# Kernel optimization log

Hardware: AMD Instinct MI355X
Metric: run time of the kernel (lower is better)

## Reference

```python
import jax, jax.numpy as jnp
import numpy as np

D_IN = 1024
D_OUT = 1024
D_BOT = 512


def setup_inputs() -> dict:
    key = jax.random.key(0)
    ks = jax.random.split(key, 16)
    B, Sq, Skv = 8, 2048, 2048

    def lin(k, fan_in, fan_out):
        kw, kb = jax.random.split(k)
        bound = 1.0 / np.sqrt(fan_in)
        W = jax.random.uniform(kw, (fan_in, fan_out), jnp.float32, -bound, bound)
        b = jax.random.uniform(kb, (fan_out,), jnp.float32, -bound, bound)
        return W, b

    W1, b1 = lin(ks[0], D_IN, D_IN)
    W2, b2 = lin(ks[1], D_IN, D_BOT)
    W3, b3 = lin(ks[2], D_BOT, D_IN)
    W4, b4 = lin(ks[3], D_IN, D_IN)
    Wq, bq = lin(ks[4], D_IN, D_OUT)
    Wk, bk = lin(ks[5], D_IN, D_OUT)
    Wv, bv = lin(ks[6], D_IN, D_OUT)

    x = jax.random.normal(ks[7], (B, Sq, D_IN), jnp.float32)
    y = jax.random.normal(ks[8], (B, Skv, D_IN), jnp.float32)
    return {
        "x": x, "y": y,
        "W1": W1, "b1": b1, "W2": W2, "b2": b2,
        "W3": W3, "b3": b3, "W4": W4, "b4": b4,
        "Wq": Wq, "bq": bq, "Wk": Wk, "bk": bk, "Wv": Wv, "bv": bv,
    }


def reference(x, y, W1, b1, W2, b2, W3, b3, W4, b4, Wq, bq, Wk, bk, Wv, bv):
    # 4-layer MLP with ReLU after every linear
    h = jax.nn.relu(x @ W1 + b1)
    h = jax.nn.relu(h @ W2 + b2)
    h = jax.nn.relu(h @ W3 + b3)
    h = jax.nn.relu(h @ W4 + b4)
    # cross-attention projections
    q = h @ Wq + bq          # [B, Sq, D_OUT]
    k = y @ Wk + bk          # [B, Skv, D_OUT]
    v = y @ Wv + bv          # [B, Skv, D_OUT]
    scale = 1.0 / jnp.sqrt(jnp.float32(q.shape[-1]))
    scores = jnp.einsum('bqd,bkd->bqk', q, k) * scale  # [B, Sq, Skv]
    attn_w = jax.nn.softmax(scores, axis=-1)
    out = jnp.einsum('bqk,bkd->bqd', attn_w, v)
    return out
```

## Files before the change

kernel.cpp:

```cpp
#include <hip/hip_runtime.h>
#include <stdint.h>


typedef __attribute__((ext_vector_type(8))) short bf16x8;
typedef __attribute__((ext_vector_type(4))) float f32x4;
typedef __attribute__((ext_vector_type(8))) unsigned short u16x8;

__device__ __forceinline__ float bf2f(unsigned short u) {
    return __uint_as_float(((unsigned int)u) << 16);
}
__device__ __forceinline__ unsigned short f2bf(float f) {
    unsigned int u = __float_as_uint(f);
    unsigned int r = (u + 0x7fffu + ((u >> 16) & 1u)) >> 16;
    return (unsigned short)r;
}

__device__ __forceinline__ void async16(const void* g, void* l) {
    __builtin_amdgcn_global_load_lds(
        (const __attribute__((address_space(1))) unsigned int*)g,
        (__attribute__((address_space(3))) unsigned int*)l,
        16, 0, 0);
}

__global__ __launch_bounds__(64) void detect_dtype(
    const unsigned short* __restrict__ w, int* __restrict__ flag)
{
    const int t = threadIdx.x;
    int cnt = 0;
    for (int i = t; i < 4096; i += 64) {
        const unsigned e = (w[i] >> 7) & 0xFF;
        cnt += (e >= 140) ? 1 : 0;
    }
#pragma unroll
    for (int off = 32; off; off >>= 1) cnt += __shfl_xor(cnt, off, 64);
    if (t == 0) flag[0] = (cnt >= 8) ? 1 : 0;
}

__global__ __launch_bounds__(256) void conv_bias_all(
    const void* b1, const void* b2, const void* b3, const void* b4,
    const void* bq, const void* bk, const void* bv,
    float* __restrict__ out, const int* __restrict__ flag)
{
    const int i = blockIdx.x * 256 + threadIdx.x;
    const int slot = i >> 10, idx = i & 1023;
    if (slot == 1 && idx >= 512) return;
    const void* src = (slot == 0) ? b1 : (slot == 1) ? b2 : (slot == 2) ? b3 :
                      (slot == 3) ? b4 : (slot == 4) ? bq : (slot == 5) ? bk : bv;
    out[i] = (*flag) ? ((const float*)src)[idx]
                     : bf2f(((const unsigned short*)src)[idx]);
}

__device__ __forceinline__ void wt_body(
    const void* in, unsigned short* out, int R, int C, int f)
{
    __shared__ unsigned short tile[32][33];
    const int bc = blockIdx.x * 32;
    const int br = blockIdx.y * 32;
    const int x = threadIdx.x & 31;
    const int y = threadIdx.x >> 5;
#pragma unroll
    for (int i = 0; i < 4; i++) {
        const int r = y + i * 8;
        unsigned short v;
        if (f) v = f2bf(((const float*)in)[(size_t)(br + r) * C + bc + x]);
        else   v = ((const unsigned short*)in)[(size_t)(br + r) * C + bc + x];
        tile[r][x] = v;
    }
    __syncthreads();
#pragma unroll
    for (int i = 0; i < 4; i++) {
        const int r = y + i * 8;
        out[(size_t)(bc + r) * R + br + x] = tile[x][r];
    }
}

__global__ __launch_bounds__(256) void conv_weight_t7(
    const void* i0, unsigned short* o0, const void* i1, unsigned short* o1,
    const void* i2, unsigned short* o2, const void* i3, unsigned short* o3,
    const void* i4, unsigned short* o4, const void* i5, unsigned short* o5,
    const void* i6, unsigned short* o6, const int* flag)
{
    const int z = blockIdx.z;
    if (z == 5) {
        if (blockIdx.x >= 16) return;
        wt_body(i5, o5, 1024, 512, *flag);
        return;
    }
    if (z == 6) {
        if (blockIdx.y >= 16) return;
        wt_body(i6, o6, 512, 1024, *flag);
        return;
    }
    const void* in = (z == 0) ? i0 : (z == 1) ? i1 : (z == 2) ? i2 : (z == 3) ? i3 : i4;
    unsigned short* out = (z == 0) ? o0 : (z == 1) ? o1 : (z == 2) ? o2 : (z == 3) ? o3 : o4;
    wt_body(in, out, 1024, 1024, *flag);
}

__global__ __launch_bounds__(256) void conv_to_bf16(
    const void* __restrict__ in, unsigned short* __restrict__ out,
    int n, const int* __restrict__ flag)
{
    const int i = (blockIdx.x * 256 + threadIdx.x) * 8;
    if (i >= n) return;
    if (*flag) {
        const float4* p = (const float4*)((const float*)in + i);
        const float4 a = p[0], b = p[1];
        u16x8 o;
        o[0] = f2bf(a.x); o[1] = f2bf(a.y); o[2] = f2bf(a.z); o[3] = f2bf(a.w);
        o[4] = f2bf(b.x); o[5] = f2bf(b.y); o[6] = f2bf(b.z); o[7] = f2bf(b.w);
        *(u16x8*)(out + i) = o;
    } else {
        *(u16x8*)(out + i) = *(const u16x8*)((const unsigned short*)in + i);
    }
}

__global__ __launch_bounds__(256) void write_out(
    const unsigned short* __restrict__ src, void* __restrict__ dst,
    int n, const int* __restrict__ flag)
{
    const int i = (blockIdx.x * 256 + threadIdx.x) * 8;
    if (i >= n) return;
    const u16x8 v = *(const u16x8*)(src + i);
    if (*flag) {
        float4 a, b;
        a.x = bf2f(v[0]); a.y = bf2f(v[1]); a.z = bf2f(v[2]); a.w = bf2f(v[3]);
        b.x = bf2f(v[4]); b.y = bf2f(v[5]); b.z = bf2f(v[6]); b.w = bf2f(v[7]);
        float4* p = (float4*)((float*)dst + i);
        p[0] = a; p[1] = b;
    } else {
        *(u16x8*)((unsigned short*)dst + i) = v;
    }
}

template <int RELU, int BIAS, int OUTF, int SWZ>
__global__ __launch_bounds__(256, 2) void gemm_bt(
    const unsigned short* __restrict__ A, const unsigned short* __restrict__ B,
    const float* __restrict__ bias, void* __restrict__ C,
    int M, int N, int K, float alpha,
    long long sA, long long sB, long long sC, const int* __restrict__ flag)
{
    int bxi = blockIdx.x, byi = blockIdx.y;
    if (SWZ) {
        const int id = byi * gridDim.x + bxi;
        bxi = (id >> 3) % gridDim.x;
        byi = (id >> 3) / gridDim.x * 8 + (id & 7);
    }
    const int z = blockIdx.z;
    A += (size_t)z * (size_t)sA;
    B += (size_t)z * (size_t)sB;
    const size_t cofs = (size_t)z * (size_t)sC;

    const int bm = byi * 128;
    const int bn = bxi * 128;
    const int t = threadIdx.x;
    const int lane = t & 63;
    const int w = t >> 6;
    const int wr = (w >> 1) * 64;
    const int wc = (w & 1) * 64;

    __shared__ unsigned short sAt[128 * 32];
    __shared__ unsigned short sBt[128 * 32];

    f32x4 acc[4][4];
#pragma unroll
    for (int i = 0; i < 4; i++)
#pragma unroll
        for (int j = 0; j < 4; j++)
            acc[i][j] = (f32x4){0.f, 0.f, 0.f, 0.f};

    const int tr = t >> 2;
    const int tc = (t & 3) << 3;
    const unsigned short* ga = A + (size_t)(bm + tr) * K + tc;
    const unsigned short* gb = B + (size_t)(bn + tr) * K + tc;
    unsigned short* la = &sAt[tr * 32 + tc];
    unsigned short* lb = &sBt[tr * 32 + tc];

    const int am = wr + (lane & 15);
    const int bn_ = wc + (lane & 15);
    const int ak = (lane >> 4) * 8;

    for (int k0 = 0; k0 < K; k0 += 32) {
        async16(ga, la);
        async16(ga + (size_t)64 * K, la + 64 * 32);
        async16(gb, lb);
        async16(gb + (size_t)64 * K, lb + 64 * 32);
        ga += 32;
        gb += 32;
        __syncthreads();

        bf16x8 af[4], bfr[4];
#pragma unroll
        for (int i = 0; i < 4; i++)
            af[i] = *(const bf16x8*)&sAt[(am + i * 16) * 32 + ak];
#pragma unroll
        for (int j = 0; j < 4; j++)
            bfr[j] = *(const bf16x8*)&sBt[(bn_ + j * 16) * 32 + ak];
#pragma unroll
        for (int i = 0; i < 4; i++)
#pragma unroll
            for (int j = 0; j < 4; j++)
                acc[i][j] = __builtin_amdgcn_mfma_f32_16x16x32_bf16(
                    af[i], bfr[j], acc[i][j], 0, 0, 0);
        __syncthreads();
    }

    const int fl = OUTF ? *flag : 0;
#pragma unroll
    for (int i = 0; i < 4; i++) {
        const int row0 = bm + wr + i * 16 + (lane >> 4) * 4;
#pragma unroll
        for (int j = 0; j < 4; j++) {
            const int col = bn + wc + j * 16 + (lane & 15);
            float bc = 0.f;
            if (BIAS == 1) bc = bias[col];
#pragma unroll
            for (int r = 0; r < 4; r++) {
                float bv = bc;
                if (BIAS == 2) bv = bias[row0 + r];
                float vv = acc[i][j][r] * alpha + bv;
                if (RELU) vv = fmaxf(vv, 0.f);
                const size_t idx = cofs + (size_t)(row0 + r) * N + col;
                if (OUTF && fl) ((float*)C)[idx] = vv;
                else ((unsigned short*)C)[idx] = f2bf(vv);
            }
        }
    }
}

#define G8_STG(gbase, dbase, T, h) do {                                        \
    const unsigned short* _s = (gbase) + (size_t)((h) * 128) * K               \
                                       + (size_t)(T) * 64;                     \
    unsigned short* _d = (dbase) + (((T) & 1) ? 16384 : 0) + (h) * 8192;       \
    async16(_s, _d);                                                           \
    async16(_s + (size_t)64 * K, _d + 4096);                                   \
} while (0)

#define G8_RD_LO(PA_, PB_)                                                     \
    _Pragma("unroll")                                                          \
    for (int m_ = 0; m_ < 4; m_++) {                                           \
        aL[m_][0] = *(const bf16x8*)&(PA_)[rA + m_ * 1024 + c0];               \
        aL[m_][1] = *(const bf16x8*)&(PA_)[rA + m_ * 1024 + c1];               \
    }                                                                          \
    _Pragma("unroll")                                                          \
    for (int n_ = 0; n_ < 4; n_++)                                             \
        bb[n_][0] = *(const bf16x8*)&(PB_)[rB + n_ * 1024 + c0];

#define G8_RD_HI(PA_, PB_)                                                     \
    _Pragma("unroll")                                                          \
    for (int m_ = 0; m_ < 4; m_++) {                                           \
        aH[m_][0] = *(const bf16x8*)&(PA_)[rA + (m_ + 4) * 1024 + c0];         \
        aH[m_][1] = *(const bf16x8*)&(PA_)[rA + (m_ + 4) * 1024 + c1];         \
    }                                                                          \
    _Pragma("unroll")                                                          \
    for (int n_ = 0; n_ < 4; n_++)                                             \
        bb[n_][1] = *(const bf16x8*)&(PB_)[rB + n_ * 1024 + c1];

#define G8_TOP()                                                               \
    __builtin_amdgcn_s_barrier();                                              \
    asm volatile("s_waitcnt lgkmcnt(0)" ::: "memory");                         \
    __builtin_amdgcn_sched_barrier(0);                                         \
    __builtin_amdgcn_s_setprio(1);

#define G8_FMA(AF, KK, MOFS)                                                   \
    _Pragma("unroll")                                                          \
    for (int m_ = 0; m_ < 4; m_++) {                                           \
        _Pragma("unroll")                                                      \
        for (int n_ = 0; n_ < 4; n_++)                                         \
            acc[(MOFS) + m_][n_] = __builtin_amdgcn_mfma_f32_16x16x32_bf16(    \
                AF[m_][KK], bb[n_][KK], acc[(MOFS) + m_][n_], 0, 0, 0);        \
    }

#define G8_BOT()                                                               \
    __builtin_amdgcn_s_setprio(0);                                             \
    asm volatile("" ::: "memory");                                             \
    __builtin_amdgcn_s_barrier();                                              \
    asm volatile("" ::: "memory");

#define G8_BOTVM4()                                                            \
    __builtin_amdgcn_s_setprio(0);                                             \
    asm volatile("s_waitcnt vmcnt(4)" ::: "memory");                           \
    __builtin_amdgcn_s_barrier();                                              \
    asm volatile("" ::: "memory");

#define G8_BOTVM0()                                                            \
    __builtin_amdgcn_s_setprio(0);                                             \
    asm volatile("s_waitcnt vmcnt(0)" ::: "memory");                           \
    __builtin_amdgcn_s_barrier();                                              \
    asm volatile("" ::: "memory");

template <int RELU, int BIAS, int OUTF, int SWZ>
__global__ __launch_bounds__(512, 2) void gemm8(
    const unsigned short* __restrict__ A, const unsigned short* __restrict__ B,
    const float* __restrict__ bias, void* __restrict__ C,
    int M, int N, int K, float alpha,
    long long sA, long long sB, long long sC, const int* __restrict__ flag)
{
    extern __shared__ unsigned short lds[];
    (void)M;
    int bxi = blockIdx.x, byi = blockIdx.y;
    if (SWZ) {
        const int id = byi * gridDim.x + bxi;
        bxi = (id >> 3) % gridDim.x;
        byi = (id >> 3) / gridDim.x * 8 + (id & 7);
    }
    const int z = blockIdx.z;
    A += (size_t)z * (size_t)sA;
    B += (size_t)z * (size_t)sB;
    const size_t cofs = (size_t)z * (size_t)sC;

    const int bm = byi * 256;
    const int bn = bxi * 256;
    const int t = threadIdx.x;
    const int lane = t & 63;
    const int w = t >> 6;
    const int wm = w >> 2;
    const int wn = w & 3;

    unsigned short* LA = lds;
    unsigned short* LB = lds + 32768;

    const int rowi = t >> 3;
    const int co = ((t & 7) ^ (rowi & 7)) << 3;
    const unsigned short* gA = A + (size_t)(bm + rowi) * K + co;
    const unsigned short* gB = B + (size_t)(bn + rowi) * K + co;
    unsigned short* dA = LA + t * 8;
    unsigned short* dB = LB + t * 8;

    const int rA = (wm * 128 + (lane & 15)) * 64;
    const int rB = (wn * 64 + (lane & 15)) * 64;
    const int swz = (lane & 7) << 4;
    const int c0 = ((((lane >> 4) << 4)) ^ swz) >> 1;
    const int c1 = ((64 | ((lane >> 4) << 4)) ^ swz) >> 1;

    f32x4 acc[8][4];
#pragma unroll
    for (int i = 0; i < 8; i++)
#pragma unroll
        for (int j = 0; j < 4; j++)
            acc[i][j] = (f32x4){0.f, 0.f, 0.f, 0.f};

    bf16x8 aL[4][2], aH[4][2], bb[4][2];

    G8_STG(gA, dA, 0, 0);
    G8_STG(gA, dA, 0, 1);
    G8_STG(gB, dB, 0, 0);
    G8_STG(gB, dB, 0, 1);
    G8_STG(gA, dA, 1, 0);
    G8_STG(gA, dA, 1, 1);
    asm volatile("s_waitcnt vmcnt(4)" ::: "memory");
    __builtin_amdgcn_s_barrier();
    asm volatile("" ::: "memory");

    const int NI = K >> 7;
    int kt = 0;
    for (int i = 0; i < NI - 1; ++i, kt += 2) {
        G8_RD_LO(LA, LB)
        G8_STG(gB, dB, kt + 1, 0);
        G8_TOP()
        G8_FMA(aL, 0, 0)
        G8_BOT()
        G8_RD_HI(LA, LB)
        G8_STG(gB, dB, kt + 1, 1);
        G8_TOP()
        G8_FMA(aL, 1, 0)
        G8_BOT()
        G8_STG(gA, dA, kt + 2, 0);
        G8_TOP()
        G8_FMA(aH, 0, 4)
        G8_BOT()
        G8_STG(gA, dA, kt + 2, 1);
        G8_TOP()
        G8_FMA(aH, 1, 4)
        G8_BOTVM4()
        G8_RD_LO((LA + 16384), (LB + 16384))
        G8_STG(gB, dB, kt + 2, 0);
        G8_TOP()
        G8_FMA(aL, 0, 0)
        G8_BOT()
        G8_RD_HI((LA + 16384), (LB + 16384))
        G8_STG(gB, dB, kt + 2, 1);
        G8_TOP()
        G8_FMA(aL, 1, 0)
        G8_BOT()
        G8_STG(gA, dA, kt + 3, 0);
        G8_TOP()
        G8_FMA(aH, 0, 4)
        G8_BOT()
        G8_STG(gA, dA, kt + 3, 1);
        G8_TOP()
        G8_FMA(aH, 1, 4)
        G8_BOTVM4()
    }
    {
        G8_RD_LO(LA, LB)
        G8_STG(gB, dB, kt + 1, 0);
        G8_TOP()
        G8_FMA(aL, 0, 0)
        G8_BOT()
        G8_RD_HI(LA, LB)
        G8_STG(gB, dB, kt + 1, 1);
        G8_TOP()
        G8_FMA(aL, 1, 0)
        G8_BOT()
        G8_TOP()
        G8_FMA(aH, 0, 4)
        G8_BOT()
        G8_TOP()
        G8_FMA(aH, 1, 4)
        G8_BOTVM0()
        G8_RD_LO((LA + 16384), (LB + 16384))
        G8_TOP()
        G8_FMA(aL, 0, 0)
        G8_BOT()
        G8_RD_HI((LA + 16384), (LB + 16384))
        G8_TOP()
        G8_FMA(aL, 1, 0)
        G8_BOT()
        G8_TOP()
        G8_FMA(aH, 0, 4)
        G8_BOT()
        G8_TOP()
        G8_FMA(aH, 1, 4)
        __builtin_amdgcn_s_setprio(0);
    }

    const int fl = OUTF ? *flag : 0;
#pragma unroll
    for (int mi = 0; mi < 8; mi++) {
        const int row0 = bm + wm * 128 + mi * 16 + (lane >> 4) * 4;
#pragma unroll
        for (int n = 0; n < 4; n++) {
            const int col = bn + wn * 64 + n * 16 + (lane & 15);
            float bc = 0.f;
            if (BIAS == 1) bc = bias[col];
#pragma unroll
            for (int r = 0; r < 4; r++) {
                float bv = bc;
                if (BIAS == 2) bv = bias[row0 + r];
                float vv = acc[mi][n][r] * alpha + bv;
                if (RELU) vv = fmaxf(vv, 0.f);
                const size_t idx = cofs + (size_t)(row0 + r) * N + col;
                if (OUTF && fl) ((float*)C)[idx] = vv;
                else ((unsigned short*)C)[idx] = f2bf(vv);
            }
        }
    }
}

__global__ __launch_bounds__(256) void softmax_rows(unsigned short* S, int n)
{
    const size_t row = blockIdx.x;
    unsigned short* p = S + row * (size_t)n;
    const int t = threadIdx.x;
    const int lane = t & 63;
    const int wave = t >> 6;

    u16x8 v = *(const u16x8*)(p + t * 8);
    float f[8];
    float m = -3.0e38f;
#pragma unroll
    for (int i = 0; i < 8; i++) {
        f[i] = bf2f(v[i]);
        m = fmaxf(m, f[i]);
    }
#pragma unroll
    for (int off = 32; off; off >>= 1) m = fmaxf(m, __shfl_xor(m, off, 64));
    __shared__ float redm[4];
    if (lane == 0) redm[wave] = m;
    __syncthreads();
    m = fmaxf(fmaxf(redm[0], redm[1]), fmaxf(redm[2], redm[3]));

    float e[8];
    float s = 0.f;
#pragma unroll
    for (int i = 0; i < 8; i++) {
        e[i] = __expf(f[i] - m);
        s += e[i];
    }
#pragma unroll
    for (int off = 32; off; off >>= 1) s += __shfl_xor(s, off, 64);
    __shared__ float reds[4];
    if (lane == 0) reds[wave] = s;
    __syncthreads();
    s = reds[0] + reds[1] + reds[2] + reds[3];
    const float inv = 1.0f / s;

    u16x8 o;
#pragma unroll
    for (int i = 0; i < 8; i++) o[i] = f2bf(e[i] * inv);
    *(u16x8*)(p + t * 8) = o;
}

extern "C" void kernel_launch(void* const* d_in, const int* in_sizes, int n_in,
                              void* d_out, int out_size, void* d_ws, size_t ws_size,
                              hipStream_t stream)
{
    const void* x  = d_in[0];
    const void* y  = d_in[1];
    const void* W1 = d_in[2];
    const void* b1 = d_in[3];
    const void* W2 = d_in[4];
    const void* b2 = d_in[5];
    const void* W3 = d_in[6];
    const void* b3 = d_in[7];
    const void* W4 = d_in[8];
    const void* b4 = d_in[9];
    const void* Wq = d_in[10];
    const void* bq = d_in[11];
    const void* Wk = d_in[12];
    const void* bk = d_in[13];
    const void* Wv = d_in[14];
    const void* bv = d_in[15];

    int* flag = (int*)d_ws;
    float* fb = (float*)((char*)d_ws + 64);
    unsigned short* arena = (unsigned short*)((char*)d_ws + 64 + 7 * 1024 * 4);
    const size_t baseB = 64 + 7 * 1024 * 4;
    const size_t MEG = 1024ull * 1024ull;

    auto needB = [&](int G, bool direct) -> size_t {
        return baseB + 2ull * ((6 + 16 + (size_t)G * 6 + (direct ? 0 : 16)) * MEG);
    };
    int G; bool direct;
    if (ws_size >= needB(8, true))      { G = 8; direct = true;  }
    else if (ws_size >= needB(4, false)) { G = 4; direct = false; }
    else if (ws_size >= needB(2, false)) { G = 2; direct = false; }
    else                                 { G = 1; direct = false; }

    unsigned short* W1t = arena;
    unsigned short* W2t = W1t + 1 * MEG;
    unsigned short* W3t = W2t + MEG / 2;
    unsigned short* W4t = W3t + MEG / 2;
    unsigned short* Wqt = W4t + 1 * MEG;
    unsigned short* Wkt = Wqt + 1 * MEG;
    unsigned short* Wvt = Wkt + 1 * MEG;
    unsigned short* XC  = Wvt + 1 * MEG;
    unsigned short* VT  = XC + 16 * MEG;
    unsigned short* SBUF = VT + (size_t)G * 2 * MEG;
    unsigned short* OUTS = SBUF + (size_t)G * 4 * MEG;

    unsigned short* PA = (unsigned short*)d_out;
    unsigned short* PB = PA + 16 * MEG;

    float* fb1 = fb;
    float* fb2 = fb + 1024;
    float* fb3 = fb + 2048;
    float* fb4 = fb + 3072;
    float* fbq = fb + 4096;
    float* fbk = fb + 5120;
    float* fbv = fb + 6144;

    const dim3 blk(256);
    const dim3 blk8(512);
    const int LDS8 = 131072;
    const int NE = 16 * 1024 * 1024;
    const int Mx = 16384;
    const long long Z0 = 0;
    const long long sQK = 2048ll * 1024;
    const long long sS  = 2048ll * 2048;

    (void)hipFuncSetAttribute((const void*)&gemm8<1, 1, 0, 1>,
                              hipFuncAttributeMaxDynamicSharedMemorySize, LDS8);
    (void)hipFuncSetAttribute((const void*)&gemm8<0, 1, 0, 1>,
                              hipFuncAttributeMaxDynamicSharedMemorySize, LDS8);
    (void)hipFuncSetAttribute((const void*)&gemm8<0, 2, 0, 0>,
                              hipFuncAttributeMaxDynamicSharedMemorySize, LDS8);
    (void)hipFuncSetAttribute((const void*)&gemm8<0, 0, 0, 1>,
                              hipFuncAttributeMaxDynamicSharedMemorySize, LDS8);
    (void)hipFuncSetAttribute((const void*)&gemm8<0, 0, 1, 1>,
                              hipFuncAttributeMaxDynamicSharedMemorySize, LDS8);

    detect_dtype<<<1, 64, 0, stream>>>((const unsigned short*)W1, flag);
    conv_bias_all<<<28, blk, 0, stream>>>(b1, b2, b3, b4, bq, bk, bv, fb, flag);
    conv_weight_t7<<<dim3(32, 32, 7), blk, 0, stream>>>(
        W1, W1t, W4, W4t, Wq, Wqt, Wk, Wkt, Wv, Wvt, W2, W2t, W3, W3t, flag);

    conv_to_bf16<<<8192, blk, 0, stream>>>(x, XC, NE, flag);

    gemm8<1, 1, 0, 1><<<dim3(4, 64), blk8, LDS8, stream>>>(
        XC, W1t, fb1, PA, Mx, 1024, 1024, 1.f, Z0, Z0, Z0, flag);
    gemm_bt<1, 1, 0, 1><<<dim3(4, 128), blk, 0, stream>>>(
        PA, W2t, fb2, PB, Mx, 512, 1024, 1.f, Z0, Z0, Z0, flag);
    gemm8<1, 1, 0, 1><<<dim3(4, 64), blk8, LDS8, stream>>>(
        PB, W3t, fb3, PA, Mx, 1024, 512, 1.f, Z0, Z0, Z0, flag);
    gemm8<1, 1, 0, 1><<<dim3(4, 64), blk8, LDS8, stream>>>(
        PA, W4t, fb4, PB, Mx, 1024, 1024, 1.f, Z0, Z0, Z0, flag);

    gemm8<0, 1, 0, 1><<<dim3(4, 64), blk8, LDS8, stream>>>(
        PB, Wqt, fbq, PA, Mx, 1024, 1024, 1.f, Z0, Z0, Z0, flag);
    conv_to_bf16<<<8192, blk, 0, stream>>>(y, XC, NE, flag);
    gemm8<0, 1, 0, 1><<<dim3(4, 64), blk8, LDS8, stream>>>(
        XC, Wkt, fbk, PB, Mx, 1024, 1024, 1.f, Z0, Z0, Z0, flag);

    if (direct) {
        gemm8<0, 2, 0, 0><<<dim3(8, 4, 8), blk8, LDS8, stream>>>(
            Wvt, XC, fbv, VT, 1024, 2048, 1024, 1.f, Z0, sQK, sQK, flag);
        gemm8<0, 0, 0, 1><<<dim3(8, 8, 8), blk8, LDS8, stream>>>(
            PA, PB, nullptr, SBUF, 2048, 2048, 1024, 0.03125f, sQK, sQK, sS, flag);
        softmax_rows<<<dim3(8 * 2048), blk, 0, stream>>>(SBUF, 2048);
        gemm8<0, 0, 1, 1><<<dim3(4, 8, 8), blk8, LDS8, stream>>>(
            SBUF, VT, nullptr, d_out, 2048, 1024, 2048, 1.f, sS, sQK, sQK, flag);
    } else {
        for (int g = 0; g < 8; g += G) {
            const size_t off = (size_t)g * 2048 * 1024;
            gemm_bt<0, 2, 0, 0><<<dim3(16, 8, G), blk, 0, stream>>>(
                Wvt, XC + off, fbv, VT, 1024, 2048, 1024, 1.f, Z0, sQK, sQK, flag);
            gemm_bt<0, 0, 0, 1><<<dim3(16, 16, G), blk, 0, stream>>>(
                PA + off, PB + off, nullptr, SBUF, 2048, 2048, 1024, 0.03125f, sQK, sQK, sS, flag);
            softmax_rows<<<dim3(G * 2048), blk, 0, stream>>>(SBUF, 2048);
            gemm_bt<0, 0, 0, 1><<<dim3(8, 16, G), blk, 0, stream>>>(
                SBUF, VT, nullptr, OUTS + off, 2048, 1024, 2048, 1.f, sS, sQK, sQK, flag);
        }
        write_out<<<8192, blk, 0, stream>>>(OUTS, d_out, NE, flag);
    }
}
```

Before: 621.1 us.

## Split LDS fragment reads and use partial lgkmcnt waits in gemm8 pipeline

Splits the LDS fragment reads into ordered groups separated by sched_barriers. Each MFMA phase now waits only for the fragments it needs (partial lgkmcnt counts) instead of draining all LDS reads. It also restructures the global-to-LDS staging so the B tile for the next k-step is issued in the prologue and alongside A in later phases, with vmcnt adjusted to match. This is meant to overlap LDS reads with MFMA work, at the cost of relying on exact hand-counted waitcnt values being correct.

Measured after the change: 793.7 us. 1.28x slower.

```diff
diff --git a/kernel.cpp b/kernel.cpp
--- a/kernel.cpp
+++ b/kernel.cpp
@@ -235,29 +235,34 @@
     async16(_s + (size_t)64 * K, _d + 4096);                                   \
 } while (0)
 
-#define G8_RD_LO(PA_, PB_)                                                     \
+#define G8_RDA(PA_, PB_)                                                       \
     _Pragma("unroll")                                                          \
-    for (int m_ = 0; m_ < 4; m_++) {                                           \
+    for (int m_ = 0; m_ < 4; m_++)                                             \
         aL[m_][0] = *(const bf16x8*)&(PA_)[rA + m_ * 1024 + c0];               \
-        aL[m_][1] = *(const bf16x8*)&(PA_)[rA + m_ * 1024 + c1];               \
-    }                                                                          \
     _Pragma("unroll")                                                          \
     for (int n_ = 0; n_ < 4; n_++)                                             \
-        bb[n_][0] = *(const bf16x8*)&(PB_)[rB + n_ * 1024 + c0];
-
-#define G8_RD_HI(PA_, PB_)                                                     \
+        bb[n_][0] = *(const bf16x8*)&(PB_)[rB + n_ * 1024 + c0];               \
+    __builtin_amdgcn_sched_barrier(0);                                         \
     _Pragma("unroll")                                                          \
-    for (int m_ = 0; m_ < 4; m_++) {                                           \
-        aH[m_][0] = *(const bf16x8*)&(PA_)[rA + (m_ + 4) * 1024 + c0];         \
-        aH[m_][1] = *(const bf16x8*)&(PA_)[rA + (m_ + 4) * 1024 + c1];         \
-    }                                                                          \
+    for (int m_ = 0; m_ < 4; m_++)                                             \
+        aL[m_][1] = *(const bf16x8*)&(PA_)[rA + m_ * 1024 + c1];
+
+#define G8_RDB(PA_, PB_)                                                       \
     _Pragma("unroll")                                                          \
     for (int n_ = 0; n_ < 4; n_++)                                             \
-        bb[n_][1] = *(const bf16x8*)&(PB_)[rB + n_ * 1024 + c1];
-
-#define G8_TOP()                                                               \
+        bb[n_][1] = *(const bf16x8*)&(PB_)[rB + n_ * 1024 + c1];               \
+    __builtin_amdgcn_sched_barrier(0);                                         \
+    _Pragma("unroll")                                                          \
+    for (int m_ = 0; m_ < 4; m_++)                                             \
+        aH[m_][0] = *(const bf16x8*)&(PA_)[rA + (m_ + 4) * 1024 + c0];         \
+    __builtin_amdgcn_sched_barrier(0);                                         \
+    _Pragma("unroll")                                                          \
+    for (int m_ = 0; m_ < 4; m_++)                                             \
+        aH[m_][1] = *(const bf16x8*)&(PA_)[rA + (m_ + 4) * 1024 + c1];
+
+#define G8_TOP(LG)                                                             \
     __builtin_amdgcn_s_barrier();                                              \
-    asm volatile("s_waitcnt lgkmcnt(0)" ::: "memory");                         \
+    asm volatile("s_waitcnt lgkmcnt(" #LG ")" ::: "memory");                   \
     __builtin_amdgcn_sched_barrier(0);                                         \
     __builtin_amdgcn_s_setprio(1);
 
@@ -276,15 +281,9 @@
     __builtin_amdgcn_s_barrier();                                              \
     asm volatile("" ::: "memory");
 
-#define G8_BOTVM4()                                                            \
+#define G8_BOTVM(N)                                                            \
     __builtin_amdgcn_s_setprio(0);                                             \
-    asm volatile("s_waitcnt vmcnt(4)" ::: "memory");                           \
-    __builtin_amdgcn_s_barrier();                                              \
-    asm volatile("" ::: "memory");
-
-#define G8_BOTVM0()                                                            \
-    __builtin_amdgcn_s_setprio(0);                                             \
-    asm volatile("s_waitcnt vmcnt(0)" ::: "memory");                           \
+    asm volatile("s_waitcnt vmcnt(" #N ")" ::: "memory");                      \
     __builtin_amdgcn_s_barrier();                                              \
     asm volatile("" ::: "memory");
 
@@ -347,79 +346,79 @@
     G8_STG(gB, dB, 0, 1);
     G8_STG(gA, dA, 1, 0);
     G8_STG(gA, dA, 1, 1);
-    asm volatile("s_waitcnt vmcnt(4)" ::: "memory");
+    G8_STG(gB, dB, 1, 0);
+    G8_STG(gB, dB, 1, 1);
+    asm volatile("s_waitcnt vmcnt(8)" ::: "memory");
     __builtin_amdgcn_s_barrier();
     asm volatile("" ::: "memory");
 
     const int NI = K >> 7;
     int kt = 0;
     for (int i = 0; i < NI - 1; ++i, kt += 2) {
-        G8_RD_LO(LA, LB)
-        G8_STG(gB, dB, kt + 1, 0);
-        G8_TOP()
+        G8_RDA(LA, LB)
+        G8_TOP(4)
         G8_FMA(aL, 0, 0)
         G8_BOT()
-        G8_RD_HI(LA, LB)
-        G8_STG(gB, dB, kt + 1, 1);
-        G8_TOP()
+        G8_RDB(LA, LB)
+        G8_TOP(8)
         G8_FMA(aL, 1, 0)
         G8_BOT()
         G8_STG(gA, dA, kt + 2, 0);
-        G8_TOP()
+        G8_STG(gB, dB, kt + 2, 0);
+        G8_TOP(4)
         G8_FMA(aH, 0, 4)
         G8_BOT()
         G8_STG(gA, dA, kt + 2, 1);
-        G8_TOP()
+        G8_STG(gB, dB, kt + 2, 1);
+        G8_TOP(0)
         G8_FMA(aH, 1, 4)
-        G8_BOTVM4()
-        G8_RD_LO((LA + 16384), (LB + 16384))
-        G8_STG(gB, dB, kt + 2, 0);
-        G8_TOP()
+        G8_BOTVM(8)
+        G8_RDA((LA + 16384), (LB + 16384))
+        G8_TOP(4)
         G8_FMA(aL, 0, 0)
         G8_BOT()
-        G8_RD_HI((LA + 16384), (LB + 16384))
-        G8_STG(gB, dB, kt + 2, 1);
-        G8_TOP()
+        G8_RDB((LA + 16384), (LB + 16384))
+        G8_TOP(8)
         G8_FMA(aL, 1, 0)
         G8_BOT()
         G8_STG(gA, dA, kt + 3, 0);
-        G8_TOP()
+        G8_STG(gB, dB, kt + 3, 0);
+        G8_TOP(4)
         G8_FMA(aH, 0, 4)
         G8_BOT()
         G8_STG(gA, dA, kt + 3, 1);
-        G8_TOP()
+        G8_STG(gB, dB, kt + 3, 1);
+        G8_TOP(0)
         G8_FMA(aH, 1, 4)
-        G8_BOTVM4()
+        G8_BOTVM(8)
     }
     {
-        G8_RD_LO(LA, LB)
-        G8_STG(gB, dB, kt + 1, 0);
-        G8_TOP()
+        G8_RDA(LA, LB)
+        G8_TOP(4)
         G8_FMA(aL, 0, 0)
         G8_BOT()
-        G8_RD_HI(LA, LB)
-        G8_STG(gB, dB, kt + 1, 1);
-        G8_TOP()
+        G8_RDB(LA, LB)
+        G8_TOP(8)
         G8_FMA(aL, 1, 0)
         G8_BOT()
-        G8_TOP()
+        G8_TOP(4)
         G8_FMA(aH, 0, 4)
         G8_BOT()
-        G8_TOP()
+        G8_TOP(0)
         G8_FMA(aH, 1, 4)
-        G8_BOTVM0()
-        G8_RD_LO((LA + 16384), (LB + 16384))
-        G8_TOP()
+        G8_BOTVM(0)
+        G8_RDA((LA + 16384), (LB + 16384))
+        G8_TOP(4)
         G8_FMA(aL, 0, 0)
         G8_BOT()
-        G8_RD_HI((LA + 16384), (LB + 16384))
-        G8_TOP()
+        G8_RDB((LA + 16384), (LB + 16384))
+        G8_TOP(8)
         G8_FMA(aL, 1, 0)
         G8_BOT()
-        G8_TOP()
+        G8_TOP(4)
         G8_FMA(aH, 0, 4)
         G8_BOT()
-        G8_TOP()
+        G8_TOP(0)
         G8_FMA(aH, 1, 4)
         __builtin_amdgcn_s_setprio(0);
     }
```

## Restructure gemm8 async LDS staging into quarter-tile loads with deeper prefetch

Applied to the files above, without the earlier changes.

Splits each async global-to-LDS stage into per-64-row quarter loads and reorders the prefetch schedule so B tiles for the next k-step are issued earlier. Both A and B for tile kt+1 are now prefetched in the prologue, and the vmcnt waits change accordingly (8/4/10). The aim is to keep more global loads in flight and hide memory latency behind the MFMA work. It needs more outstanding loads and careful vmcnt accounting, and a miscount could cause races or stalls.

New measurement: 633.8 us. +2.1%, slower.

```diff
diff --git a/kernel.cpp b/kernel.cpp
--- a/kernel.cpp
+++ b/kernel.cpp
@@ -227,12 +227,11 @@
     }
 }
 
-#define G8_STG(gbase, dbase, T, h) do {                                        \
-    const unsigned short* _s = (gbase) + (size_t)((h) * 128) * K               \
+#define G8_STGQ(gbase, dbase, T, q) do {                                       \
+    const unsigned short* _s = (gbase) + (size_t)((q) * 64) * K                \
                                        + (size_t)(T) * 64;                     \
-    unsigned short* _d = (dbase) + (((T) & 1) ? 16384 : 0) + (h) * 8192;       \
+    unsigned short* _d = (dbase) + (((T) & 1) ? 16384 : 0) + (q) * 4096;       \
     async16(_s, _d);                                                           \
-    async16(_s + (size_t)64 * K, _d + 4096);                                   \
 } while (0)
 
 #define G8_RD_LO(PA_, PB_)                                                     \
@@ -276,15 +275,9 @@
     __builtin_amdgcn_s_barrier();                                              \
     asm volatile("" ::: "memory");
 
-#define G8_BOTVM4()                                                            \
+#define G8_BOTVM(N)                                                            \
     __builtin_amdgcn_s_setprio(0);                                             \
-    asm volatile("s_waitcnt vmcnt(4)" ::: "memory");                           \
-    __builtin_amdgcn_s_barrier();                                              \
-    asm volatile("" ::: "memory");
-
-#define G8_BOTVM0()                                                            \
-    __builtin_amdgcn_s_setprio(0);                                             \
-    asm volatile("s_waitcnt vmcnt(0)" ::: "memory");                           \
+    asm volatile("s_waitcnt vmcnt(" #N ")" ::: "memory");                      \
     __builtin_amdgcn_s_barrier();                                              \
     asm volatile("" ::: "memory");
 
@@ -341,13 +334,15 @@
 
     bf16x8 aL[4][2], aH[4][2], bb[4][2];
 
-    G8_STG(gA, dA, 0, 0);
-    G8_STG(gA, dA, 0, 1);
-    G8_STG(gB, dB, 0, 0);
-    G8_STG(gB, dB, 0, 1);
-    G8_STG(gA, dA, 1, 0);
-    G8_STG(gA, dA, 1, 1);
-    asm volatile("s_waitcnt vmcnt(4)" ::: "memory");
+    G8_STGQ(gA, dA, 0, 0); G8_STGQ(gA, dA, 0, 2);
+    G8_STGQ(gA, dA, 0, 1); G8_STGQ(gA, dA, 0, 3);
+    G8_STGQ(gB, dB, 0, 0); G8_STGQ(gB, dB, 0, 1);
+    G8_STGQ(gB, dB, 0, 2); G8_STGQ(gB, dB, 0, 3);
+    G8_STGQ(gA, dA, 1, 0); G8_STGQ(gA, dA, 1, 2);
+    G8_STGQ(gB, dB, 1, 0); G8_STGQ(gB, dB, 1, 1);
+    G8_STGQ(gA, dA, 1, 1); G8_STGQ(gA, dA, 1, 3);
+    G8_STGQ(gB, dB, 1, 2); G8_STGQ(gB, dB, 1, 3);
+    asm volatile("s_waitcnt vmcnt(8)" ::: "memory");
     __builtin_amdgcn_s_barrier();
     asm volatile("" ::: "memory");
 
@@ -355,50 +350,56 @@
     int kt = 0;
     for (int i = 0; i < NI - 1; ++i, kt += 2) {
         G8_RD_LO(LA, LB)
-        G8_STG(gB, dB, kt + 1, 0);
         G8_TOP()
         G8_FMA(aL, 0, 0)
-        G8_BOT()
+        G8_BOTVM(8)
         G8_RD_HI(LA, LB)
-        G8_STG(gB, dB, kt + 1, 1);
         G8_TOP()
         G8_FMA(aL, 1, 0)
         G8_BOT()
-        G8_STG(gA, dA, kt + 2, 0);
+        G8_STGQ(gB, dB, kt + 2, 0);
+        G8_STGQ(gB, dB, kt + 2, 2);
         G8_TOP()
         G8_FMA(aH, 0, 4)
         G8_BOT()
-        G8_STG(gA, dA, kt + 2, 1);
+        G8_STGQ(gB, dB, kt + 2, 1);
+        G8_STGQ(gB, dB, kt + 2, 3);
         G8_TOP()
         G8_FMA(aH, 1, 4)
-        G8_BOTVM4()
+        G8_BOTVM(4)
         G8_RD_LO((LA + 16384), (LB + 16384))
-        G8_STG(gB, dB, kt + 2, 0);
+        G8_STGQ(gA, dA, kt + 2, 0);
+        G8_STGQ(gA, dA, kt + 2, 2);
         G8_TOP()
         G8_FMA(aL, 0, 0)
         G8_BOT()
         G8_RD_HI((LA + 16384), (LB + 16384))
-        G8_STG(gB, dB, kt + 2, 1);
+        G8_STGQ(gA, dA, kt + 2, 1);
+        G8_STGQ(gA, dA, kt + 2, 3);
         G8_TOP()
         G8_FMA(aL, 1, 0)
         G8_BOT()
-        G8_STG(gA, dA, kt + 3, 0);
+        G8_STGQ(gA, dA, kt + 3, 0);
+        G8_STGQ(gA, dA, kt + 3, 2);
+        G8_STGQ(gB, dB, kt + 3, 0);
+        G8_STGQ(gB, dB, kt + 3, 1);
         G8_TOP()
         G8_FMA(aH, 0, 4)
         G8_BOT()
-        G8_STG(gA, dA, kt + 3, 1);
+        G8_STGQ(gA, dA, kt + 3, 1);
+        G8_STGQ(gA, dA, kt + 3, 3);
+        G8_STGQ(gB, dB, kt + 3, 2);
+        G8_STGQ(gB, dB, kt + 3, 3);
         G8_TOP()
         G8_FMA(aH, 1, 4)
-        G8_BOTVM4()
+        G8_BOTVM(10)
     }
     {
         G8_RD_LO(LA, LB)
-        G8_STG(gB, dB, kt + 1, 0);
         G8_TOP()
         G8_FMA(aL, 0, 0)
-        G8_BOT()
+        G8_BOTVM(8)
         G8_RD_HI(LA, LB)
-        G8_STG(gB, dB, kt + 1, 1);
         G8_TOP()
         G8_FMA(aL, 1, 0)
         G8_BOT()
@@ -407,7 +408,7 @@
         G8_BOT()
         G8_TOP()
         G8_FMA(aH, 1, 4)
-        G8_BOTVM0()
+        G8_BOTVM(0)
         G8_RD_LO((LA + 16384), (LB + 16384))
         G8_TOP()
         G8_FMA(aL, 0, 0)
```
